# Optimization experiments

Hardware: AMD Instinct MI355X
Metric: run time of the kernel (lower is better)

Reference implementation:

```python
import jax, jax.numpy as jnp
import numpy as np
import itertools

N_GRAPHS = 64
NODES_PER_GRAPH = 16
N_NODES = N_GRAPHS * NODES_PER_GRAPH  # 1024


def conv2d(x, w, b, stride=1):
    # x: [N, Cin, H, W], w: [Cout, Cin, 3, 3], padding=1 (same as torch Conv2d(...,3,stride,1))
    y = jax.lax.conv_general_dilated(
        x, w, (stride, stride), ((1, 1), (1, 1)),
        dimension_numbers=("NCHW", "OIHW", "NCHW"))
    return y + b[None, :, None, None]


def lrelu(x):
    return jax.nn.leaky_relu(x, 0.1)


def conv_mpn(x, edges, c1w, c1b, c2w, c2b, c3w, c3b):
    # ConvMPN: gather neighbour / non-neighbour node features, scatter_add to dst,
    # concat on channel dim, then 3 convs (no activation in between, as in source).
    n = x.shape[0]
    a, s, b = edges[:, 0], edges[:, 1], edges[:, 2]
    src = jnp.concatenate([a, b])  # bidirectional, matches torch cat([e0,e2]) / cat([e2,e0])
    dst = jnp.concatenate([b, a])
    pos = jnp.concatenate([s > 0, s > 0]).astype(x.dtype)
    neg = jnp.concatenate([s < 0, s < 0]).astype(x.dtype)
    gathered = x[src]  # [2E, C, H, W]
    neigh = jax.ops.segment_sum(gathered * pos[:, None, None, None], dst, num_segments=n)
    non = jax.ops.segment_sum(gathered * neg[:, None, None, None], dst, num_segments=n)
    h = jnp.concatenate([x, neigh, non], axis=1)  # [N, 3C, H, W]
    h = conv2d(h, c1w, c1b)
    h = conv2d(h, c2w, c2b)
    h = conv2d(h, c3w, c3b)
    return h


def setup_inputs() -> dict:
    key = jax.random.key(0)
    ks = iter(jax.random.split(key, 40))

    def p(shape):
        fan_in = int(np.prod(shape[1:])) if len(shape) > 1 else shape[0]
        return jax.random.normal(next(ks), shape, dtype=jnp.float32) / np.sqrt(fan_in)

    x = jax.random.normal(next(ks), (N_NODES, 32, 32), dtype=jnp.float32)
    t = jax.random.normal(next(ks), (N_NODES, 10), dtype=jnp.float32)

    # complete graph per sample; sign +/-1 marks neighbour vs non-neighbour
    pairs = np.array(list(itertools.combinations(range(NODES_PER_GRAPH), 2)))  # (120, 2)
    offs = np.arange(N_GRAPHS)[:, None] * NODES_PER_GRAPH
    aa = (pairs[None, :, 0] + offs).ravel()
    bb = (pairs[None, :, 1] + offs).ravel()
    rng = np.random.RandomState(0)
    sign = rng.choice(np.array([-1, 1]), size=aa.shape[0])
    edges = jnp.asarray(np.stack([aa, sign, bb], axis=1).astype(np.int64))
    nd_to_sample = jnp.asarray(np.repeat(np.arange(N_GRAPHS), NODES_PER_GRAPH).astype(np.int64))

    inp = {
        "x": x, "t": t, "edges": edges, "nd_to_sample": nd_to_sample,
        "w_t": p((8192, 10)), "b_t": jnp.zeros((8192,), jnp.float32),
        "c1w": p((16, 9, 3, 3)), "c1b": jnp.zeros((16,), jnp.float32),
        "c2w": p((16, 16, 3, 3)), "c2b": jnp.zeros((16,), jnp.float32),
        "c3w": p((16, 16, 3, 3)), "c3b": jnp.zeros((16,), jnp.float32),
        "m1c1w": p((32, 48, 3, 3)), "m1c1b": jnp.zeros((32,), jnp.float32),
        "m1c2w": p((32, 32, 3, 3)), "m1c2b": jnp.zeros((32,), jnp.float32),
        "m1c3w": p((16, 32, 3, 3)), "m1c3b": jnp.zeros((16,), jnp.float32),
        "ds1w": p((16, 16, 3, 3)), "ds1b": jnp.zeros((16,), jnp.float32),
        "m2c1w": p((32, 48, 3, 3)), "m2c1b": jnp.zeros((32,), jnp.float32),
        "m2c2w": p((32, 32, 3, 3)), "m2c2b": jnp.zeros((32,), jnp.float32),
        "m2c3w": p((16, 32, 3, 3)), "m2c3b": jnp.zeros((16,), jnp.float32),
        "ds2w": p((16, 16, 3, 3)), "ds2b": jnp.zeros((16,), jnp.float32),
        "d1w": p((256, 16, 3, 3)), "d1b": jnp.zeros((256,), jnp.float32),
        "d2w": p((128, 256, 3, 3)), "d2b": jnp.zeros((128,), jnp.float32),
        "d3w": p((128, 128, 3, 3)), "d3b": jnp.zeros((128,), jnp.float32),
        "pw": p((1, 128)), "pb": jnp.zeros((1,), jnp.float32),
    }
    return inp


def reference(x, t, edges, nd_to_sample,
              w_t, b_t, c1w, c1b, c2w, c2b, c3w, c3b,
              m1c1w, m1c1b, m1c2w, m1c2b, m1c3w, m1c3b, ds1w, ds1b,
              m2c1w, m2c1b, m2c2w, m2c2b, m2c3w, m2c3b, ds2w, ds2b,
              d1w, d1b, d2w, d2b, d3w, d3b, pw, pb):
    h = x.reshape(-1, 1, 32, 32)
    tt = (t @ w_t.T + b_t).reshape(-1, 8, 32, 32)
    h = jnp.concatenate([h, tt], axis=1)  # [N, 9, 32, 32]
    h = lrelu(conv2d(h, c1w, c1b))
    h = lrelu(conv2d(h, c2w, c2b))
    h = lrelu(conv2d(h, c3w, c3b))
    h = conv_mpn(h, edges, m1c1w, m1c1b, m1c2w, m1c2b, m1c3w, m1c3b)
    h = lrelu(conv2d(h, ds1w, ds1b, stride=2))  # 32 -> 16
    h = conv_mpn(h, edges, m2c1w, m2c1b, m2c2w, m2c2b, m2c3w, m2c3b)
    h = lrelu(conv2d(h, ds2w, ds2b, stride=2))  # 16 -> 8
    h = lrelu(conv2d(h, d1w, d1b, stride=2))    # 8 -> 4
    h = lrelu(conv2d(h, d2w, d2b, stride=2))    # 4 -> 2
    h = lrelu(conv2d(h, d3w, d3b, stride=2))    # 2 -> 1
    h = h.reshape(-1, h.shape[1])               # [N, 128]
    pooled = jax.ops.segment_sum(h, nd_to_sample, num_segments=N_GRAPHS)  # add_pool
    return pooled @ pw.T + pb                    # [B, 1]
```

## Files before the change

### kernel.cpp

```cpp
#include <hip/hip_runtime.h>
#include <hip/hip_bf16.h>


#define N_NODES   1024
#define N_GRAPHS  64

typedef __hip_bfloat16 bf16;
typedef __attribute__((ext_vector_type(8)))  short  short8;
typedef __attribute__((ext_vector_type(16))) float  f32x16;

__device__ __forceinline__ float bf2f(unsigned short s) {
    union { unsigned u; float f; } x; x.u = ((unsigned)s) << 16; return x.f;
}
__device__ __forceinline__ unsigned cvtpk(float a, float b) {
    unsigned r;
    asm("v_cvt_pk_bf16_f32 %0, %1, %2" : "=v"(r) : "v"(a), "v"(b));
    return r;
}
__device__ __forceinline__ uint4 pack8(const float* f) {
    uint4 r;
    r.x = cvtpk(f[0], f[1]);
    r.y = cvtpk(f[2], f[3]);
    r.z = cvtpk(f[4], f[5]);
    r.w = cvtpk(f[6], f[7]);
    return r;
}
__device__ __forceinline__ void gload16(const void* g, void* l) {
    __builtin_amdgcn_global_load_lds(
        reinterpret_cast<const __attribute__((address_space(1))) unsigned*>(
            reinterpret_cast<uintptr_t>(g)),
        reinterpret_cast<__attribute__((address_space(3))) unsigned*>(
            reinterpret_cast<uintptr_t>(l)),
        16, 0, 0);
}

template<int N>
__device__ __forceinline__ void zacc(f32x16* a) {
    #pragma unroll
    for (int i = 0; i < N; ++i)
        #pragma unroll
        for (int e = 0; e < 16; ++e) a[i][e] = 0.f;
}

template<int WIN, int WOUT, int STRIDE, int TPW, int TILES, int NW>
__device__ __forceinline__ void mfma_phase(
    const short* lds, int inbase, int zch,
    const unsigned short* wfb, int kkstride_sh,
    f32x16* acc, int wid, int lane)
{
    constexpr int NPI = WIN * WIN;
    const int pxl = lane & 31, kg = lane >> 5;
    short8 wfr[9];
    #pragma unroll
    for (int kk = 0; kk < 9; ++kk)
        wfr[kk] = *(const short8*)(wfb + (size_t)kk * kkstride_sh + lane * 8);
    #pragma unroll
    for (int kk = 0; kk < 9; ++kk) {
        #pragma unroll
        for (int t = 0; t < TPW; ++t) {
            int tile = wid * TPW + t;
            if (NW * TPW > TILES && tile >= TILES) continue;
            int oy, ox;
            if (WOUT == 32)      { oy = tile;                  ox = pxl;      }
            else if (WOUT == 16) { oy = tile * 2 + (pxl >> 4); ox = pxl & 15; }
            else                 { oy = tile * 4 + (pxl >> 3); ox = pxl & 7;  }
            int iy = STRIDE * oy + kk / 3 - 1, ix = STRIDE * ox + kk % 3 - 1;
            bool ok = ((unsigned)iy < (unsigned)WIN) && ((unsigned)ix < (unsigned)WIN);
            int chunk = ok ? (inbase + kg * NPI + iy * WIN + ix) : zch;
            acc[t] = __builtin_amdgcn_mfma_f32_32x32x16_bf16(
                wfr[kk], *(const short8*)(lds + (size_t)chunk * 8), acc[t], 0, 0, 0);
        }
    }
}

template<int WOUT, int COUT, int RELU, int TPW, int TILES, int NW, bool TOGLOBAL>
__device__ __forceinline__ void conv_epi(
    short* lds, int outbase, unsigned short* gout,
    const float* __restrict__ bias, const f32x16* acc, int wid, int lane)
{
    constexpr int NPO = WOUT * WOUT;
    const int pxl = lane & 31, kg = lane >> 5;
    #pragma unroll
    for (int t = 0; t < TPW; ++t) {
        int tile = wid * TPW + t;
        if (NW * TPW > TILES && tile >= TILES) continue;
        int oy, ox;
        if (WOUT == 32)      { oy = tile;                  ox = pxl;      }
        else if (WOUT == 16) { oy = tile * 2 + (pxl >> 4); ox = pxl & 15; }
        else                 { oy = tile * 4 + (pxl >> 3); ox = pxl & 7;  }
        int opx = oy * WOUT + ox;
        #pragma unroll
        for (int q = 0; q < COUT / 8; ++q) {
            float v[4];
            #pragma unroll
            for (int j = 0; j < 4; ++j) {
                int co = q * 8 + kg * 4 + j;
                float x = acc[t][4 * q + j] + bias[co];
                v[j] = RELU ? ((x >= 0.f) ? x : 0.1f * x) : x;
            }
            uint2 pk;
            pk.x = cvtpk(v[0], v[1]);
            pk.y = cvtpk(v[2], v[3]);
            if constexpr (TOGLOBAL)
                *(uint2*)(gout + ((size_t)q * NPO + opx) * 8 + kg * 4) = pk;
            else
                *(uint2*)(lds + ((size_t)(outbase + q * NPO + opx)) * 8 + kg * 4) = pk;
        }
    }
}

#define N_PREP 14
struct PrepArgs {
    const float* w[N_PREP];
    unsigned short* o[N_PREP];
    int cin[N_PREP], cout[N_PREP], cig[N_PREP], mt[N_PREP], base[N_PREP];
    int prep_total;
    const int* edges; int per_g;
    int* adj_cnt; int* adj_lst;
    float* out; const float* pb;
};

__global__ __launch_bounds__(64) void k_setup(PrepArgs a)
{
    int b = blockIdx.x;
    int tid = threadIdx.x;
    if (b < a.prep_total) {
        int L = 0;
        #pragma unroll
        for (int i = 1; i < N_PREP; ++i) if (b >= a.base[i]) L = i;
        int rel = b - a.base[L];
        int MT = a.mt[L], CIG = a.cig[L];
        int m = rel % MT; rel /= MT;
        int cg = rel % CIG;
        int kk = rel / CIG;
        int Cin = a.cin[L], Cout = a.cout[L];
        int co = m * 32 + (tid & 31), kg = tid >> 5;
        float v[8];
        #pragma unroll
        for (int j = 0; j < 8; ++j) {
            int ci = cg * 16 + kg * 8 + j;
            v[j] = (co < Cout && ci < Cin) ? a.w[L][((size_t)co * Cin + ci) * 9 + kk] : 0.f;
        }
        *(uint4*)(a.o[L] + ((size_t)((kk * CIG + cg) * MT + m) * 64 + tid) * 8) = pack8(v);
    } else if (b < a.prep_total + 16) {
        int n = (b - a.prep_total) * 64 + tid;
        int g = n >> 4;
        const int* eg = a.edges + (size_t)g * a.per_g * 3;
        int c = 0;
        for (int k = 0; k < a.per_g; ++k) {
            int aa = eg[k * 3 + 0];
            int s  = eg[k * 3 + 1];
            int bb = eg[k * 3 + 2];
            int other = (aa == n) ? bb : ((bb == n) ? aa : -1);
            if (other >= 0 && (other >> 4) == g && c < 16) {
                a.adj_lst[n * 16 + c] = other | ((s < 0) ? (int)0x80000000 : 0);
                ++c;
            }
        }
        a.adj_cnt[n] = c;
    } else {
        if (tid < N_GRAPHS) a.out[tid] = a.pb[0];
    }
}

__global__ __launch_bounds__(512) void k_front(
    const float* __restrict__ x, const float* __restrict__ t,
    const float* __restrict__ wt, const float* __restrict__ bt,
    const unsigned short* __restrict__ wf1, const float* __restrict__ b1,
    const unsigned short* __restrict__ wf2, const float* __restrict__ b2,
    const unsigned short* __restrict__ wf3, const float* __restrict__ b3,
    bf16* __restrict__ c3o, int node_base)
{
    __shared__ __align__(16) short lds[4097 * 8];
    __shared__ float s_t[10];
    const int nl = blockIdx.x, n = node_base + nl, tid = threadIdx.x;
    const int wid = tid >> 6, lane = tid & 63;
    if (tid < 10) s_t[tid] = t[n * 10 + tid];
    if (tid < 8)  lds[4096 * 8 + tid] = 0;
    __syncthreads();

    #pragma unroll
    for (int p = 0; p < 2; ++p) {
        int px = tid + p * 512;
        float ch[16];
        ch[0] = x[(size_t)n * 1024 + px];
        #pragma unroll
        for (int c = 1; c <= 8; ++c) {
            int o = (c - 1) * 1024 + px;
            float a = bt[o];
            const float* wr = wt + (size_t)o * 10;
            #pragma unroll
            for (int k = 0; k < 10; ++k) a += wr[k] * s_t[k];
            ch[c] = a;
        }
        #pragma unroll
        for (int c = 9; c < 16; ++c) ch[c] = 0.f;
        *(uint4*)(lds + (size_t)px * 8)          = pack8(ch);
        *(uint4*)(lds + (size_t)(1024 + px) * 8) = pack8(ch + 8);
    }
    __syncthreads();

    f32x16 acc[4];
    zacc<4>(acc);
    mfma_phase<32, 32, 1, 4, 32, 8>(lds, 0, 4096, wf1, 512, acc, wid, lane);
    conv_epi<32, 16, 1, 4, 32, 8, false>(lds, 2048, nullptr, b1, acc, wid, lane);
    __syncthreads();
    zacc<4>(acc);
    mfma_phase<32, 32, 1, 4, 32, 8>(lds, 2048, 4096, wf2, 512, acc, wid, lane);
    conv_epi<32, 16, 1, 4, 32, 8, false>(lds, 0, nullptr, b2, acc, wid, lane);
    __syncthreads();
    zacc<4>(acc);
    mfma_phase<32, 32, 1, 4, 32, 8>(lds, 0, 4096, wf3, 512, acc, wid, lane);
    conv_epi<32, 16, 1, 4, 32, 8, true>(lds, 0,
        (unsigned short*)c3o + (size_t)nl * 16384, b3, acc, wid, lane);
}

__global__ __launch_bounds__(512) void k_mid1(
    const bf16* __restrict__ c3o, const bf16* __restrict__ g1p,
    const unsigned short* __restrict__ wf1, const float* __restrict__ b1,
    const unsigned short* __restrict__ wf2, const float* __restrict__ b2,
    const unsigned short* __restrict__ wf3, const float* __restrict__ b3,
    const unsigned short* __restrict__ wfd, const float* __restrict__ bd,
    bf16* __restrict__ ds1o)
{
    __shared__ __align__(16) short lds[8193 * 8];
    const int nl = blockIdx.x, tid = threadIdx.x;
    const int wid = tid >> 6, lane = tid & 63;
    if (tid < 8) lds[8192 * 8 + tid] = 0;

    uint4* l4 = (uint4*)lds;
    const uint4* s0 = (const uint4*)c3o + (size_t)nl * 2048;
    const uint4* s1 = (const uint4*)g1p + (size_t)nl * 4096;
    const uint4* s2 = s1 + 2048;
    #pragma unroll
    for (int r = 0; r < 4; ++r) l4[tid + r * 512] = s0[tid + r * 512];
    __syncthreads();

    f32x16 acc[4];
    zacc<4>(acc);
    uint4 pf[4];
    #pragma unroll
    for (int r = 0; r < 4; ++r) pf[r] = s1[tid + r * 512];
    mfma_phase<32, 32, 1, 4, 32, 8>(lds, 0, 8192, wf1, 3 * 512, acc, wid, lane);
    #pragma unroll
    for (int r = 0; r < 4; ++r) l4[2048 + tid + r * 512] = pf[r];
    __syncthreads();
    #pragma unroll
    for (int r = 0; r < 4; ++r) pf[r] = s2[tid + r * 512];
    mfma_phase<32, 32, 1, 4, 32, 8>(lds, 2048, 8192, wf1 + 512, 3 * 512, acc, wid, lane);
    #pragma unroll
    for (int r = 0; r < 4; ++r) l4[tid + r * 512] = pf[r];
    __syncthreads();
    mfma_phase<32, 32, 1, 4, 32, 8>(lds, 0, 8192, wf1 + 1024, 3 * 512, acc, wid, lane);
    conv_epi<32, 32, 0, 4, 32, 8, false>(lds, 4096, nullptr, b1, acc, wid, lane);
    __syncthreads();

    zacc<4>(acc);
    mfma_phase<32, 32, 1, 4, 32, 8>(lds, 4096, 8192, wf2,       2 * 512, acc, wid, lane);
    mfma_phase<32, 32, 1, 4, 32, 8>(lds, 6144, 8192, wf2 + 512, 2 * 512, acc, wid, lane);
    conv_epi<32, 32, 0, 4, 32, 8, false>(lds, 0, nullptr, b2, acc, wid, lane);
    __syncthreads();

    zacc<4>(acc);
    mfma_phase<32, 32, 1, 4, 32, 8>(lds, 0,    8192, wf3,       2 * 512, acc, wid, lane);
    mfma_phase<32, 32, 1, 4, 32, 8>(lds, 2048, 8192, wf3 + 512, 2 * 512, acc, wid, lane);
    conv_epi<32, 16, 0, 4, 32, 8, false>(lds, 4096, nullptr, b3, acc, wid, lane);
    __syncthreads();

    zacc<1>(acc);
    mfma_phase<32, 16, 2, 1, 8, 8>(lds, 4096, 8192, wfd, 512, acc, wid, lane);
    conv_epi<16, 16, 1, 1, 8, 8, true>(lds, 0,
        (unsigned short*)ds1o + (size_t)nl * 4096, bd, acc, wid, lane);
}

__global__ __launch_bounds__(512) void k_mid2(
    const bf16* __restrict__ ds1o, const bf16* __restrict__ g2p,
    const unsigned short* __restrict__ wf1, const float* __restrict__ b1,
    const unsigned short* __restrict__ wf2, const float* __restrict__ b2,
    const unsigned short* __restrict__ wf3, const float* __restrict__ b3,
    const unsigned short* __restrict__ wfd, const float* __restrict__ bd,
    bf16* __restrict__ ds2o)
{
    __shared__ __align__(16) short lds[2049 * 8];
    const int nl = blockIdx.x, tid = threadIdx.x;
    const int wid = tid >> 6, lane = tid & 63;
    if (tid < 8) lds[2048 * 8 + tid] = 0;

    uint4* l4 = (uint4*)lds;
    const uint4* s0 = (const uint4*)ds1o + (size_t)nl * 512;
    const uint4* s1 = (const uint4*)g2p + (size_t)nl * 1024;
    const uint4* s2 = s1 + 512;
    l4[tid] = s0[tid];
    __syncthreads();

    f32x16 acc[1];
    zacc<1>(acc);
    uint4 pf;
    pf = s1[tid];
    mfma_phase<16, 16, 1, 1, 8, 8>(lds, 0, 2048, wf1, 3 * 512, acc, wid, lane);
    l4[512 + tid] = pf;
    __syncthreads();
    pf = s2[tid];
    mfma_phase<16, 16, 1, 1, 8, 8>(lds, 512, 2048, wf1 + 512, 3 * 512, acc, wid, lane);
    l4[tid] = pf;
    __syncthreads();
    mfma_phase<16, 16, 1, 1, 8, 8>(lds, 0, 2048, wf1 + 1024, 3 * 512, acc, wid, lane);
    conv_epi<16, 32, 0, 1, 8, 8, false>(lds, 1024, nullptr, b1, acc, wid, lane);
    __syncthreads();

    zacc<1>(acc);
    mfma_phase<16, 16, 1, 1, 8, 8>(lds, 1024, 2048, wf2,       2 * 512, acc, wid, lane);
    mfma_phase<16, 16, 1, 1, 8, 8>(lds, 1536, 2048, wf2 + 512, 2 * 512, acc, wid, lane);
    conv_epi<16, 32, 0, 1, 8, 8, false>(lds, 0, nullptr, b2, acc, wid, lane);
    __syncthreads();

    zacc<1>(acc);
    mfma_phase<16, 16, 1, 1, 8, 8>(lds, 0,   2048, wf3,       2 * 512, acc, wid, lane);
    mfma_phase<16, 16, 1, 1, 8, 8>(lds, 512, 2048, wf3 + 512, 2 * 512, acc, wid, lane);
    conv_epi<16, 16, 0, 1, 8, 8, false>(lds, 1024, nullptr, b3, acc, wid, lane);
    __syncthreads();

    zacc<1>(acc);
    mfma_phase<16, 8, 2, 1, 2, 8>(lds, 1024, 2048, wfd, 512, acc, wid, lane);
    conv_epi<8, 16, 1, 1, 2, 8, true>(lds, 0,
        (unsigned short*)ds2o + (size_t)nl * 1024, bd, acc, wid, lane);
}

template<int NPIX>
__global__ __launch_bounds__(256) void k_gather2(
    const bf16* __restrict__ in, const int* __restrict__ cnt,
    const int* __restrict__ lst, bf16* __restrict__ out, int node_base)
{
    constexpr int CPN = 2 * NPIX;
    __shared__ __align__(16) uint4 s_in[16 * 128];
    __shared__ int s_pos[16], s_neg[16];

    const int gl = blockIdx.x, sp = blockIdx.y, tid = threadIdx.x;
    const int gn0 = node_base + gl * 16, nl0 = gl * 16;

    if (tid < 16) {
        int c = cnt[gn0 + tid]; if (c > 16) c = 16;
        int pm = 0, nm = 0;
        for (int k = 0; k < c; ++k) {
            int e = lst[(size_t)(gn0 + tid) * 16 + k];
            int sl = (e & 0x7FFFFFFF) - gn0;
            if ((unsigned)sl < 16u) { if (e < 0) nm |= 1 << sl; else pm |= 1 << sl; }
        }
        s_pos[tid] = pm; s_neg[tid] = nm;
    }
    const uint4* in4 = (const uint4*)in;
    #pragma unroll
    for (int k = 0; k < 8; ++k) {
        int i = tid + k * 256;
        int srcn = i >> 7, chk = i & 127;
        gload16(&in4[(size_t)(nl0 + srcn) * CPN + sp * 128 + chk], &s_in[i]);
    }
    __syncthreads();

    const int dh = tid >> 7, ch = tid & 127;
    int pm[8], nm[8];
    #pragma unroll
    for (int dl = 0; dl < 8; ++dl) {
        pm[dl] = __builtin_amdgcn_readfirstlane(s_pos[dh * 8 + dl]);
        nm[dl] = __builtin_amdgcn_readfirstlane(s_neg[dh * 8 + dl]);
    }

    float aP[8][8], aN[8][8];
    #pragma unroll
    for (int dl = 0; dl < 8; ++dl)
        #pragma unroll
        for (int j = 0; j < 8; ++j) { aP[dl][j] = 0.f; aN[dl][j] = 0.f; }

    for (int s = 0; s < 16; ++s) {
        union { uint4 v; unsigned short u[8]; } q;
        q.v = s_in[s * 128 + ch];
        float f[8];
        #pragma unroll
        for (int j = 0; j < 8; ++j) f[j] = bf2f(q.u[j]);
        #pragma unroll
        for (int dl = 0; dl < 8; ++dl) {
            if ((pm[dl] >> s) & 1) {
                #pragma unroll
                for (int j = 0; j < 8; ++j) aP[dl][j] += f[j];
            }
            if ((nm[dl] >> s) & 1) {
                #pragma unroll
                for (int j = 0; j < 8; ++j) aN[dl][j] += f[j];
            }
        }
    }

    uint4* out4 = (uint4*)out;
    #pragma unroll
    for (int dl = 0; dl < 8; ++dl) {
        int d = nl0 + dh * 8 + dl;
        out4[((size_t)d * 2 + 0) * CPN + sp * 128 + ch] = pack8(aP[dl]);
        out4[((size_t)d * 2 + 1) * CPN + sp * 128 + ch] = pack8(aN[dl]);
    }
}

__global__ __launch_bounds__(512) void k_tail3(
    const bf16* __restrict__ ds2o,
    const unsigned short* __restrict__ w1, const float* __restrict__ b1,
    const unsigned short* __restrict__ w2, const float* __restrict__ b2,
    const unsigned short* __restrict__ w3, const float* __restrict__ b3,
    const int* __restrict__ nd, const float* __restrict__ pw,
    float* __restrict__ out, int node_base)
{
    __shared__ __align__(16) short lds[5121 * 8];
    __shared__ float s_part[4][8];
    const int tid = threadIdx.x, wid = tid >> 6, lane = tid & 63;
    const int col = lane & 31, kg = lane >> 5;
    const int img0 = blockIdx.x * 8;
    if (tid < 8) lds[5120 * 8 + tid] = 0;

    const uint4* src = (const uint4*)ds2o + (size_t)img0 * 128;
    gload16(src + tid,       (uint4*)lds + tid);
    gload16(src + 512 + tid, (uint4*)lds + 512 + tid);
    __syncthreads();

    {
        f32x16 acc[4];
        zacc<4>(acc);
        #pragma unroll
        for (int t = 0; t < 4; ++t) {
            int tl = wid + 8 * t;
            int m = tl >> 2, n = tl & 3;
            int idx = n * 32 + col;
            int img = idx >> 4, px = idx & 15;
            int oy = px >> 2, ox = px & 3;
            #pragma unroll
            for (int kk = 0; kk < 9; ++kk) {
                int iy = 2 * oy + kk / 3 - 1, ix = 2 * ox + kk % 3 - 1;
                bool ok = ((unsigned)iy < 8u) && ((unsigned)ix < 8u);
                int chunk = ok ? (img * 128 + kg * 64 + iy * 8 + ix) : 5120;
                short8 wfr = *(const short8*)(w1 + ((size_t)(kk * 8 + m) * 64 + lane) * 8);
                acc[t] = __builtin_amdgcn_mfma_f32_32x32x16_bf16(
                    wfr, *(const short8*)(lds + (size_t)chunk * 8), acc[t], 0, 0, 0);
            }
        }
        #pragma unroll
        for (int t = 0; t < 4; ++t) {
            int tl = wid + 8 * t;
            int m = tl >> 2, n = tl & 3;
            int idx = n * 32 + col;
            int img = idx >> 4, px = idx & 15;
            #pragma unroll
            for (int q = 0; q < 4; ++q) {
                float v[4];
                #pragma unroll
                for (int j = 0; j < 4; ++j) {
                    int co = m * 32 + q * 8 + kg * 4 + j;
                    float x = acc[t][4 * q + j] + b1[co];
                    v[j] = (x >= 0.f) ? x : 0.1f * x;
                }
                uint2 pk;
                pk.x = cvtpk(v[0], v[1]);
                pk.y = cvtpk(v[2], v[3]);
                *(uint2*)(lds + ((size_t)(1024 + img * 512 + (m * 4 + q) * 16 + px)) * 8
                          + kg * 4) = pk;
            }
        }
    }
    __syncthreads();

    {
        f32x16 acc;
        #pragma unroll
        for (int e = 0; e < 16; ++e) acc[e] = 0.f;
        int img = col >> 2, px = col & 3;
        int oy = px >> 1, ox = px & 1;
        int poff[9];
        #pragma unroll
        for (int kk = 0; kk < 9; ++kk) {
            int iy = 2 * oy + kk / 3 - 1, ix = 2 * ox + kk % 3 - 1;
            bool ok = ((unsigned)iy < 4u) && ((unsigned)ix < 4u);
            poff[kk] = ok ? (iy * 4 + ix) : -1;
        }
        if (wid < 4) {
            for (int cig = 0; cig < 16; ++cig) {
                #pragma unroll
                for (int kk = 0; kk < 9; ++kk) {
                    short8 wfr = *(const short8*)(w2 +
                        ((size_t)((kk * 16 + cig) * 4 + wid) * 64 + lane) * 8);
                    int chunk = (poff[kk] >= 0)
                              ? 1024 + img * 512 + (cig * 2 + kg) * 16 + poff[kk]
                              : 5120;
                    acc = __builtin_amdgcn_mfma_f32_32x32x16_bf16(
                        wfr, *(const short8*)(lds + (size_t)chunk * 8), acc, 0, 0, 0);
                }
            }
        }
        __syncthreads();
        if (wid < 4) {
            #pragma unroll
            for (int q = 0; q < 4; ++q) {
                float v[4];
                #pragma unroll
                for (int j = 0; j < 4; ++j) {
                    int co = wid * 32 + q * 8 + kg * 4 + j;
                    float x = acc[4 * q + j] + b2[co];
                    v[j] = (x >= 0.f) ? x : 0.1f * x;
                }
                uint2 pk;
                pk.x = cvtpk(v[0], v[1]);
                pk.y = cvtpk(v[2], v[3]);
                *(uint2*)(lds + ((size_t)(img * 64 + (wid * 4 + q) * 4 + px)) * 8
                          + kg * 4) = pk;
            }
        }
    }
    __syncthreads();

    {
        if (wid < 4) {
            int img = col;
            bool live = col < 8;
            f32x16 acc;
            #pragma unroll
            for (int e = 0; e < 16; ++e) acc[e] = 0.f;
            for (int cig = 0; cig < 8; ++cig) {
                #pragma unroll
                for (int kk = 0; kk < 9; ++kk) {
                    int iy = kk / 3 - 1, ix = kk % 3 - 1;
                    bool ok = live && ((unsigned)iy < 2u) && ((unsigned)ix < 2u);
                    int chunk = ok ? (img * 64 + (cig * 2 + kg) * 4 + iy * 2 + ix) : 5120;
                    short8 wfr = *(const short8*)(w3 +
                        ((size_t)((kk * 8 + cig) * 4 + wid) * 64 + lane) * 8);
                    acc = __builtin_amdgcn_mfma_f32_32x32x16_bf16(
                        wfr, *(const short8*)(lds + (size_t)chunk * 8), acc, 0, 0, 0);
                }
            }
            float part = 0.f;
            #pragma unroll
            for (int r = 0; r < 16; ++r) {
                int co = wid * 32 + (r & 3) + 8 * (r >> 2) + 4 * kg;
                float v = acc[r] + b3[co];
                v = (v >= 0.f) ? v : 0.1f * v;
                part += v * pw[co];
            }
            part += __shfl_xor(part, 32, 64);
            if (kg == 0 && live) s_part[wid][col] = part;
        }
        __syncthreads();
        if (tid < 8) {
            float s = s_part[0][tid] + s_part[1][tid] + s_part[2][tid] + s_part[3][tid];
            int g = nd[node_base + img0 + tid];
            if (g < 0) g = 0; if (g >= N_GRAPHS) g = N_GRAPHS - 1;
            atomicAdd(&out[g], s);
        }
    }
}

extern "C" void kernel_launch(void* const* d_in, const int* in_sizes, int n_in,
                              void* d_out, int out_size, void* d_ws, size_t ws_size,
                              hipStream_t stream)
{
    const float* x     = (const float*)d_in[0];
    const float* t     = (const float*)d_in[1];
    const int*   edges = (const int*)d_in[2];
    const int*   nd    = (const int*)d_in[3];
    const float* w_t   = (const float*)d_in[4];
    const float* b_t   = (const float*)d_in[5];
    const float* c1w   = (const float*)d_in[6];
    const float* c1b   = (const float*)d_in[7];
    const float* c2w   = (const float*)d_in[8];
    const float* c2b   = (const float*)d_in[9];
    const float* c3w   = (const float*)d_in[10];
    const float* c3b   = (const float*)d_in[11];
    const float* m1c1w = (const float*)d_in[12];
    const float* m1c1b = (const float*)d_in[13];
    const float* m1c2w = (const float*)d_in[14];
    const float* m1c2b = (const float*)d_in[15];
    const float* m1c3w = (const float*)d_in[16];
    const float* m1c3b = (const float*)d_in[17];
    const float* ds1w  = (const float*)d_in[18];
    const float* ds1b  = (const float*)d_in[19];
    const float* m2c1w = (const float*)d_in[20];
    const float* m2c1b = (const float*)d_in[21];
    const float* m2c2w = (const float*)d_in[22];
    const float* m2c2b = (const float*)d_in[23];
    const float* m2c3w = (const float*)d_in[24];
    const float* m2c3b = (const float*)d_in[25];
    const float* ds2w  = (const float*)d_in[26];
    const float* ds2b  = (const float*)d_in[27];
    const float* d1w   = (const float*)d_in[28];
    const float* d1b   = (const float*)d_in[29];
    const float* d2w   = (const float*)d_in[30];
    const float* d2b   = (const float*)d_in[31];
    const float* d3w   = (const float*)d_in[32];
    const float* d3b   = (const float*)d_in[33];
    const float* pw    = (const float*)d_in[34];
    const float* pb    = (const float*)d_in[35];
    float* out = (float*)d_out;

    uint8_t* ws = (uint8_t*)d_ws;
    int* adj_cnt = (int*)ws;
    int* adj_lst = (int*)(ws + 4096);
    #define WF(i)  ((unsigned short*)(ws + (128u << 10) + (size_t)(i) * 32768))
    unsigned short* wt_ds1 = (unsigned short*)(ws + (416u  << 10));
    unsigned short* wt_ds2 = (unsigned short*)(ws + (428u  << 10));
    unsigned short* wt_d1  = (unsigned short*)(ws + (440u  << 10));
    unsigned short* wt_d2  = (unsigned short*)(ws + (512u  << 10));
    unsigned short* wt_d3  = (unsigned short*)(ws + (1088u << 10));

    const size_t RESV = 2ull << 20;
    size_t avail = (ws_size > RESV) ? ws_size - RESV : 0;
    int ncap = (int)(avail / (104 * 1024));
    ncap = (ncap / 16) * 16;
    if (ncap < 16) ncap = 16;
    if (ncap > N_NODES) ncap = N_NODES;
    uint8_t* R = ws + RESV;
    #define NB(off_kb) (R + (size_t)(off_kb) * 1024 * ncap)

    bf16*  c3o  = (bf16*)NB(0);
    bf16*  g1p  = (bf16*)NB(32);
    bf16*  ds1o = (bf16*)NB(96);
    bf16*  g2p  = (bf16*)NB(0);
    bf16*  ds2o = (bf16*)NB(16);

    int nE    = in_sizes[2] / 3;
    int per_g = nE / N_GRAPHS;

    {
        PrepArgs pa;
        const float* wsrc[N_PREP] = { c1w, c2w, c3w, m1c1w, m1c2w, m1c3w,
                                      m2c1w, m2c2w, m2c3w, ds1w, ds2w,
                                      d1w, d2w, d3w };
        unsigned short* wdst[N_PREP] = { WF(0), WF(1), WF(2), WF(3), WF(4), WF(5),
                                         WF(6), WF(7), WF(8), wt_ds1, wt_ds2,
                                         wt_d1, wt_d2, wt_d3 };
        int cin_[N_PREP]  = { 9, 16, 16, 48, 32, 32, 48, 32, 32, 16, 16, 16, 256, 128 };
        int cout_[N_PREP] = { 16, 16, 16, 32, 32, 16, 32, 32, 16, 16, 16, 256, 128, 128 };
        int cig_[N_PREP]  = { 1, 1, 1, 3, 2, 2, 3, 2, 2, 1, 1, 1, 16, 8 };
        int mt_[N_PREP]   = { 1, 1, 1, 1, 1, 1, 1, 1, 1, 1, 1, 8, 4, 4 };
        int total = 0;
        for (int i = 0; i < N_PREP; ++i) {
            pa.w[i] = wsrc[i]; pa.o[i] = wdst[i];
            pa.cin[i] = cin_[i]; pa.cout[i] = cout_[i];
            pa.cig[i] = cig_[i]; pa.mt[i] = mt_[i];
            pa.base[i] = total;
            total += 9 * cig_[i] * mt_[i];
        }
        pa.prep_total = total;
        pa.edges = edges; pa.per_g = per_g;
        pa.adj_cnt = adj_cnt; pa.adj_lst = adj_lst;
        pa.out = out; pa.pb = pb;
        k_setup<<<total + 16 + 1, 64, 0, stream>>>(pa);
    }

    for (int nb = 0; nb < N_NODES; nb += ncap) {
        int nc = (N_NODES - nb < ncap) ? (N_NODES - nb) : ncap;
        int ng = nc / 16;

        k_front<<<nc, 512, 0, stream>>>(x, t, w_t, b_t,
            WF(0), c1b, WF(1), c2b, WF(2), c3b, c3o, nb);

        k_gather2<1024><<<dim3(ng, 16), 256, 0, stream>>>(c3o, adj_cnt, adj_lst, g1p, nb);

        k_mid1<<<nc, 512, 0, stream>>>(c3o, g1p,
            WF(3), m1c1b, WF(4), m1c2b, WF(5), m1c3b, wt_ds1, ds1b, ds1o);

        k_gather2<256><<<dim3(ng, 4), 256, 0, stream>>>(ds1o, adj_cnt, adj_lst, g2p, nb);

        k_mid2<<<nc, 512, 0, stream>>>(ds1o, g2p,
            WF(6), m2c1b, WF(7), m2c2b, WF(8), m2c3b, wt_ds2, ds2b, ds2o);

        k_tail3<<<nc / 8, 512, 0, stream>>>(ds2o,
            wt_d1, d1b, wt_d2, d2b, wt_d3, d3b, nd, pw, out, nb);
    }
    #undef NB
    #undef WF
}
```

Baseline: 249.5 us.

## Split mid1 fused conv chain into two row halves with halo recompute

The fused MPN conv chain plus downsample kernel is split into two blocks per node, each handling half of the image rows with overlapping halo rows that are recomputed through the three 3x3 convs. This halves LDS use per block (about 76KB to 38KB) so more blocks can be resident per CU and doubles the grid. Input staging now uses async global-to-LDS loads, and each stage is fenced by a barrier instead of register prefetch overlapped with MFMA. The cost is redundant halo computation (about 10-20% extra MFMA work) and more synchronisation.

```diff
diff --git a/kernel.cpp b/kernel.cpp
--- a/kernel.cpp
+++ b/kernel.cpp
@@ -105,6 +105,59 @@
                 *(uint2*)(gout + ((size_t)q * NPO + opx) * 8 + kg * 4) = pk;
             else
                 *(uint2*)(lds + ((size_t)(outbase + q * NPO + opx)) * 8 + kg * 4) = pk;
+        }
+    }
+}
+
+__device__ __forceinline__ void mfma_rows(
+    const short* lds, int inbase, int gstride, int zch,
+    const unsigned short* wfb, int kkstride_sh,
+    f32x16* acc, int wid, int lane, int or0, int orn, int ir0)
+{
+    const int pxl = lane & 31, kg = lane >> 5;
+    short8 wfr[9];
+    #pragma unroll
+    for (int kk = 0; kk < 9; ++kk)
+        wfr[kk] = *(const short8*)(wfb + (size_t)kk * kkstride_sh + lane * 8);
+    #pragma unroll
+    for (int kk = 0; kk < 9; ++kk) {
+        #pragma unroll
+        for (int t = 0; t < 3; ++t) {
+            int tile = wid * 3 + t;
+            if (tile >= orn) continue;
+            int oy = or0 + tile;
+            int iy = oy + kk / 3 - 1, ix = pxl + kk % 3 - 1;
+            bool ok = ((unsigned)iy < 32u) && ((unsigned)ix < 32u);
+            int chunk = ok ? (inbase + kg * gstride + (iy - ir0) * 32 + ix) : zch;
+            acc[t] = __builtin_amdgcn_mfma_f32_32x32x16_bf16(
+                wfr[kk], *(const short8*)(lds + (size_t)chunk * 8), acc[t], 0, 0, 0);
+        }
+    }
+}
+
+__device__ __forceinline__ void epi_rows(
+    short* lds, int outbase, int sstride, int gstride,
+    const float* __restrict__ bias, const f32x16* acc,
+    int wid, int lane, int or0, int orn, int nq)
+{
+    const int pxl = lane & 31, kg = lane >> 5;
+    #pragma unroll
+    for (int t = 0; t < 3; ++t) {
+        int tile = wid * 3 + t;
+        if (tile >= orn) continue;
+        int lr = tile;
+        for (int q = 0; q < nq; ++q) {
+            float v[4];
+            #pragma unroll
+            for (int j = 0; j < 4; ++j) {
+                int co = q * 8 + kg * 4 + j;
+                v[j] = acc[t][4 * q + j] + bias[co];
+            }
+            uint2 pk;
+            pk.x = cvtpk(v[0], v[1]);
+            pk.y = cvtpk(v[2], v[3]);
+            *(uint2*)(lds + ((size_t)(outbase + (q >> 1) * sstride + (q & 1) * gstride
+                      + lr * 32 + pxl)) * 8 + kg * 4) = pk;
         }
     }
 }
@@ -215,7 +268,7 @@
         (unsigned short*)c3o + (size_t)nl * 16384, b3, acc, wid, lane);
 }
 
-__global__ __launch_bounds__(512) void k_mid1(
+__global__ __launch_bounds__(512) void k_mid1h(
     const bf16* __restrict__ c3o, const bf16* __restrict__ g1p,
     const unsigned short* __restrict__ wf1, const float* __restrict__ b1,
     const unsigned short* __restrict__ wf2, const float* __restrict__ b2,
@@ -223,54 +276,110 @@
     const unsigned short* __restrict__ wfd, const float* __restrict__ bd,
     bf16* __restrict__ ds1o)
 {
-    __shared__ __align__(16) short lds[8193 * 8];
-    const int nl = blockIdx.x, tid = threadIdx.x;
+    __shared__ __align__(16) short lds[4737 * 8];
+    const int nl = blockIdx.x, h = blockIdx.y, tid = threadIdx.x;
     const int wid = tid >> 6, lane = tid & 63;
-    if (tid < 8) lds[8192 * 8 + tid] = 0;
-
-    uint4* l4 = (uint4*)lds;
-    const uint4* s0 = (const uint4*)c3o + (size_t)nl * 2048;
-    const uint4* s1 = (const uint4*)g1p + (size_t)nl * 4096;
-    const uint4* s2 = s1 + 2048;
-    #pragma unroll
-    for (int r = 0; r < 4; ++r) l4[tid + r * 512] = s0[tid + r * 512];
-    __syncthreads();
-
-    f32x16 acc[4];
-    zacc<4>(acc);
-    uint4 pf[4];
-    #pragma unroll
-    for (int r = 0; r < 4; ++r) pf[r] = s1[tid + r * 512];
-    mfma_phase<32, 32, 1, 4, 32, 8>(lds, 0, 8192, wf1, 3 * 512, acc, wid, lane);
-    #pragma unroll
-    for (int r = 0; r < 4; ++r) l4[2048 + tid + r * 512] = pf[r];
-    __syncthreads();
-    #pragma unroll
-    for (int r = 0; r < 4; ++r) pf[r] = s2[tid + r * 512];
-    mfma_phase<32, 32, 1, 4, 32, 8>(lds, 2048, 8192, wf1 + 512, 3 * 512, acc, wid, lane);
-    #pragma unroll
-    for (int r = 0; r < 4; ++r) l4[tid + r * 512] = pf[r];
-    __syncthreads();
-    mfma_phase<32, 32, 1, 4, 32, 8>(lds, 0, 8192, wf1 + 1024, 3 * 512, acc, wid, lane);
-    conv_epi<32, 32, 0, 4, 32, 8, false>(lds, 4096, nullptr, b1, acc, wid, lane);
-    __syncthreads();
-
-    zacc<4>(acc);
-    mfma_phase<32, 32, 1, 4, 32, 8>(lds, 4096, 8192, wf2,       2 * 512, acc, wid, lane);
-    mfma_phase<32, 32, 1, 4, 32, 8>(lds, 6144, 8192, wf2 + 512, 2 * 512, acc, wid, lane);
-    conv_epi<32, 32, 0, 4, 32, 8, false>(lds, 0, nullptr, b2, acc, wid, lane);
-    __syncthreads();
-
-    zacc<4>(acc);
-    mfma_phase<32, 32, 1, 4, 32, 8>(lds, 0,    8192, wf3,       2 * 512, acc, wid, lane);
-    mfma_phase<32, 32, 1, 4, 32, 8>(lds, 2048, 8192, wf3 + 512, 2 * 512, acc, wid, lane);
-    conv_epi<32, 16, 0, 4, 32, 8, false>(lds, 4096, nullptr, b3, acc, wid, lane);
-    __syncthreads();
-
-    zacc<1>(acc);
-    mfma_phase<32, 16, 2, 1, 8, 8>(lds, 4096, 8192, wfd, 512, acc, wid, lane);
-    conv_epi<16, 16, 1, 1, 8, 8, true>(lds, 0,
-        (unsigned short*)ds1o + (size_t)nl * 4096, bd, acc, wid, lane);
+    const int pxl = lane & 31, kg = lane >> 5;
+    if (tid < 8) lds[4736 * 8 + tid] = 0;
+
+    const int in_r0 = h ? 12 : 0;
+    const int c1_r0 = h ? 13 : 0, orn1 = h ? 19 : 18;
+    const int c2_r0 = h ? 14 : 0, orn2 = h ? 18 : 17;
+    const int c3_r0 = h ? 15 : 0, orn3 = h ? 17 : 16;
+
+    constexpr int P0 = 0,    PS = 2 * 19 * 32, PG = 19 * 32;
+    constexpr int S0 = 2432, SG = 20 * 32;
+    constexpr int Q0 = 2432, QS = 2 * 18 * 32, QG = 18 * 32;
+    constexpr int C0 = 0,    CG = 17 * 32;
+    constexpr int ZCH = 4736;
+
+    const uint4* selfp = (const uint4*)c3o + (size_t)nl * 2048;
+    const uint4* posp  = (const uint4*)g1p + (size_t)nl * 4096;
+    const uint4* negp  = posp + 2048;
+
+    #define STAGE(srcbase)                                                    \
+        {                                                                     \
+            int i0 = tid;          gload16((srcbase) + (i0 < 640 ? i0 : 384 + i0), \
+                                           (uint4*)lds + S0 + i0);            \
+            int i1 = tid + 512;    gload16((srcbase) + (i1 < 640 ? i1 : 384 + i1), \
+                                           (uint4*)lds + S0 + i1);            \
+            if (tid < 256) {                                                  \
+                int i2 = tid + 1024;                                          \
+                gload16((srcbase) + 384 + i2, (uint4*)lds + S0 + i2);         \
+            }                                                                 \
+        }
+
+    const uint4* s_self = selfp + in_r0 * 32;
+    const uint4* s_pos  = posp  + in_r0 * 32;
+    const uint4* s_neg  = negp  + in_r0 * 32;
+
+    f32x16 acc[3];
+    zacc<3>(acc);
+
+    STAGE(s_self);
+    __syncthreads();
+    mfma_rows(lds, S0, SG, ZCH, wf1,        3 * 512, acc, wid, lane, c1_r0, orn1, in_r0);
+    __syncthreads();
+    STAGE(s_pos);
+    __syncthreads();
+    mfma_rows(lds, S0, SG, ZCH, wf1 + 512,  3 * 512, acc, wid, lane, c1_r0, orn1, in_r0);
+    __syncthreads();
+    STAGE(s_neg);
+    __syncthreads();
+    mfma_rows(lds, S0, SG, ZCH, wf1 + 1024, 3 * 512, acc, wid, lane, c1_r0, orn1, in_r0);
+    epi_rows(lds, P0, PS, PG, b1, acc, wid, lane, c1_r0, orn1, 4);
+    __syncthreads();
+
+    zacc<3>(acc);
+    mfma_rows(lds, P0,      PG, ZCH, wf2,       2 * 512, acc, wid, lane, c2_r0, orn2, c1_r0);
+    mfma_rows(lds, P0 + PS, PG, ZCH, wf2 + 512, 2 * 512, acc, wid, lane, c2_r0, orn2, c1_r0);
+    epi_rows(lds, Q0, QS, QG, b2, acc, wid, lane, c2_r0, orn2, 4);
+    __syncthreads();
+
+    zacc<3>(acc);
+    mfma_rows(lds, Q0,      QG, ZCH, wf3,       2 * 512, acc, wid, lane, c3_r0, orn3, c2_r0);
+    mfma_rows(lds, Q0 + QS, QG, ZCH, wf3 + 512, 2 * 512, acc, wid, lane, c3_r0, orn3, c2_r0);
+    epi_rows(lds, C0, 0, CG, b3, acc, wid, lane, c3_r0, orn3, 2);
+    __syncthreads();
+
+    {
+        f32x16 a0;
+        #pragma unroll
+        for (int e = 0; e < 16; ++e) a0[e] = 0.f;
+        short8 wfr[9];
+        #pragma unroll
+        for (int kk = 0; kk < 9; ++kk)
+            wfr[kk] = *(const short8*)(wfd + (size_t)kk * 512 + lane * 8);
+        if (wid < 4) {
+            int oy = 8 * h + wid * 2 + (pxl >> 4);
+            int ox = pxl & 15;
+            #pragma unroll
+            for (int kk = 0; kk < 9; ++kk) {
+                int iy = 2 * oy + kk / 3 - 1, ix = 2 * ox + kk % 3 - 1;
+                bool ok = ((unsigned)iy < 32u) && ((unsigned)ix < 32u);
+                int chunk = ok ? (C0 + kg * CG + (iy - c3_r0) * 32 + ix) : ZCH;
+                a0 = __builtin_amdgcn_mfma_f32_32x32x16_bf16(
+                    wfr[kk], *(const short8*)(lds + (size_t)chunk * 8), a0, 0, 0, 0);
+            }
+            unsigned short* gout = (unsigned short*)ds1o + (size_t)nl * 4096;
+            int opx = oy * 16 + ox;
+            #pragma unroll
+            for (int q = 0; q < 2; ++q) {
+                float v[4];
+                #pragma unroll
+                for (int j = 0; j < 4; ++j) {
+                    int co = q * 8 + kg * 4 + j;
+                    float xx = a0[4 * q + j] + bd[co];
+                    v[j] = (xx >= 0.f) ? xx : 0.1f * xx;
+                }
+                uint2 pk;
+                pk.x = cvtpk(v[0], v[1]);
+                pk.y = cvtpk(v[2], v[3]);
+                *(uint2*)(gout + ((size_t)q * 256 + opx) * 8 + kg * 4) = pk;
+            }
+        }
+    }
+    #undef STAGE
 }
 
 __global__ __launch_bounds__(512) void k_mid2(
@@ -658,7 +767,7 @@
 
         k_gather2<1024><<<dim3(ng, 16), 256, 0, stream>>>(c3o, adj_cnt, adj_lst, g1p, nb);
 
-        k_mid1<<<nc, 512, 0, stream>>>(c3o, g1p,
+        k_mid1h<<<dim3(nc, 2), 512, 0, stream>>>(c3o, g1p,
             WF(3), m1c1b, WF(4), m1c2b, WF(5), m1c3b, wt_ds1, ds1b, ds1o);
 
         k_gather2<256><<<dim3(ng, 4), 256, 0, stream>>>(ds1o, adj_cnt, adj_lst, g2p, nb);
```

Measured after the change: 276.2 us. 1.11x slower.
